# Optimization experiments

Measured on AMD Instinct MI355X. Metric: run time of the kernel, lower is better.

Reference implementation:

```python
import jax, jax.numpy as jnp
import numpy as np

K = 8  # args.k


def setup_inputs() -> dict:
    key = jax.random.key(0)
    k1, k2, k3 = jax.random.split(key, 3)
    b, n_pre, n_cur = 1, 8192, 16384
    pre_xyzs = jax.random.normal(k1, (b, 3, n_pre), dtype=jnp.float32)
    cur_xyzs = jax.random.normal(k2, (b, 3, n_cur), dtype=jnp.float32)
    # UpsampleNumLayer output range: sigmoid * (max_upsample_num - 1) + 1  in [1, 8]
    upsample_num = jax.random.uniform(k3, (b, n_pre), dtype=jnp.float32) * 7.0 + 1.0
    return {"pre_xyzs": pre_xyzs, "cur_xyzs": cur_xyzs, "upsample_num": upsample_num}


def _sqdist(a, b):
    # a: (b, n, 3), b: (b, m, 3) -> (b, n, m) squared euclidean distances
    return ((a * a).sum(-1)[:, :, None]
            + (b * b).sum(-1)[:, None, :]
            - 2.0 * jnp.einsum('bnc,bmc->bnm', a, b))


def reference(pre_xyzs, cur_xyzs, upsample_num):
    # pre_xyzs: (b, 3, n_pre); cur_xyzs: (b, 3, n_cur); upsample_num: (b, n_pre)
    pre_t = pre_xyzs.transpose(0, 2, 1)  # (b, n_pre, 3)
    cur_t = cur_xyzs.transpose(0, 2, 1)  # (b, n_cur, 3)

    # knnquery_heap(1, pre, cur): nearest pre index for each cur point -> (b, n_cur)
    cur2pre = jnp.argmin(_sqdist(cur_t, pre_t), axis=-1)

    # knnquery_heap(K, cur, pre): K nearest cur indices for each pre point -> (b, n_pre, K)
    _, knn_idx = jax.lax.top_k(-_sqdist(pre_t, cur_t), K)

    # real_center: gather cur2pre at knn_idx -> (b, n_pre, K)
    real_center = jax.vmap(lambda c2p, idx: c2p[idx])(cur2pre, knn_idx)
    expect_center = jnp.arange(pre_xyzs.shape[2])[None, :, None]  # (1, n_pre, 1)
    mask = (expect_center == real_center).astype(pre_xyzs.dtype)  # (b, n_pre, K)

    # knn_xyzs: gather cur_xyzs columns at knn_idx -> (b, 3, n_pre, K)
    knn_xyzs = jax.vmap(lambda pts, idx: pts[:, idx])(cur_xyzs, knn_idx)

    diff = knn_xyzs - pre_xyzs[..., None]              # (b, 3, n_pre, K)
    dist = jnp.sqrt((diff * diff).sum(axis=1))         # (b, n_pre, K), L2 over channel dim
    mean_distance = (dist * mask).sum(axis=-1) / upsample_num  # (b, n_pre)
    return mean_distance
```

## Files before the change

### kernel.cpp

```cpp
#include <hip/hip_runtime.h>

#define N_PRE 8192
#define N_CUR 16384
#define KNN   8


#define MAPPED_INF 0xFF800000u

__device__ __forceinline__ unsigned key_of_bits(unsigned b) {
    return b ^ (0x80000000u | (unsigned)((int)b >> 31));
}
__device__ __forceinline__ float float_of_key(unsigned k) {
    unsigned b = k ^ (0x80000000u | ~(unsigned)((int)k >> 31));
    return __uint_as_float(b);
}

__global__ __launch_bounds__(256) void prep_kernel(
        const float* __restrict__ pre, const float* __restrict__ cur,
        float4* __restrict__ pre4, float4* __restrict__ cur4) {
    int i = blockIdx.x * 256 + threadIdx.x;
    if (i < N_CUR) {
        float x = cur[i], y = cur[N_CUR + i], z = cur[2 * N_CUR + i];
        cur4[i] = make_float4(x, y, z, fmaf(x, x, fmaf(y, y, z * z)));
    }
    if (i < N_PRE) {
        float x = pre[i], y = pre[N_PRE + i], z = pre[2 * N_PRE + i];
        pre4[i] = make_float4(-2.f * x, -2.f * y, -2.f * z,
                              fmaf(x, x, fmaf(y, y, z * z)));
    }
}

#define TILE_A 2048

__global__ __launch_bounds__(1024) void cur2pre_kernel(
        const float4* __restrict__ pre4, const float4* __restrict__ cur4,
        unsigned* __restrict__ c2p) {
    __shared__ float4 sp[TILE_A];
    const int tid  = threadIdx.x;
    const int lane = tid & 63;
    const int w    = tid >> 6;
    const int j0   = blockIdx.x * 32 + w * 2;

    const float4 c0 = cur4[j0 + 0];
    const float4 c1 = cur4[j0 + 1];

    const float INF = __int_as_float(0x7F800000);
    float b0 = INF, b1 = INF;
    int   i0 = 0,   i1 = 0;

    for (int tile = 0; tile < N_PRE; tile += TILE_A) {
        __syncthreads();
        for (int k = tid; k < TILE_A; k += 1024) sp[k] = pre4[tile + k];
        __syncthreads();

#pragma unroll 8
        for (int s = 0; s < TILE_A; s += 64) {
            float4 q = sp[s + lane];
            int idx = tile + s + lane;
            float d; bool c;
            d = fmaf(q.x, c0.x, fmaf(q.y, c0.y, fmaf(q.z, c0.z, q.w)));
            c = d < b0; b0 = c ? d : b0; i0 = c ? idx : i0;
            d = fmaf(q.x, c1.x, fmaf(q.y, c1.y, fmaf(q.z, c1.z, q.w)));
            c = d < b1; b1 = c ? d : b1; i1 = c ? idx : i1;
        }
    }

    unsigned long long v0 =
        (((unsigned long long)key_of_bits(__float_as_uint(b0))) << 32) | (unsigned)i0;
    unsigned long long v1 =
        (((unsigned long long)key_of_bits(__float_as_uint(b1))) << 32) | (unsigned)i1;
#pragma unroll
    for (int off = 32; off > 0; off >>= 1) {
        unsigned long long o;
        o = __shfl_xor(v0, off); v0 = (o < v0) ? o : v0;
        o = __shfl_xor(v1, off); v1 = (o < v1) ? o : v1;
    }
    unsigned r = (unsigned)v0;
    r = (lane == 1) ? (unsigned)v1 : r;
    if (lane < 2) c2p[j0 + lane] = r;
}

#define TILE_B 1024

__device__ __forceinline__ void pop_top8(float d, float& t8, unsigned& ld,
                                         unsigned& li, int jbase) {
    unsigned long long m = __ballot(d < t8);
    while (m) {
        int src = __ffsll(m) - 1;
        unsigned fdb = (unsigned)__builtin_amdgcn_readlane(__float_as_int(d), src);
        unsigned kd = key_of_bits(fdb);
        unsigned kj = (unsigned)(jbase + src);
        unsigned ud = (unsigned)__builtin_amdgcn_update_dpp(
            0, (int)ld, 0x111, 0xF, 0xF, false);
        unsigned uj = (unsigned)__builtin_amdgcn_update_dpp(
            0, (int)li, 0x111, 0xF, 0xF, false);
        bool hi = kd < ud;
        bool lo = kd < ld;
        ld = hi ? ud : (lo ? kd : ld);
        li = hi ? uj : (lo ? kj : li);
        unsigned k7 = (unsigned)__builtin_amdgcn_readlane((int)ld, 7);
        t8 = float_of_key(k7);
        m = (m & (m - 1)) & __ballot(d < t8);
    }
}

__global__ __launch_bounds__(512) void knn_finalize_kernel(
        const float4* __restrict__ pre4, const float4* __restrict__ cur4,
        const float* __restrict__ ups,
        const unsigned* __restrict__ c2p,
        float* __restrict__ out) {
    __shared__ float4 sc[2 * TILE_B];
    unsigned long long* mb = (unsigned long long*)sc;

    const int tid  = threadIdx.x;
    const int lane = tid & 63;
    const int w    = tid >> 6;
    const int half = w >> 2;
    const int wl   = w & 3;
    const int ia   = blockIdx.x * 8 + wl * 2;
    const int ib   = ia + 1;
    const int hbase = half * (N_CUR / 2);

    const float4 p0 = pre4[ia];
    const float4 p1 = pre4[ib];

    const float INF = __int_as_float(0x7F800000);
    unsigned ld0 = MAPPED_INF, li0 = 0, ld1 = MAPPED_INF, li1 = 0;
    float t80 = INF, t81 = INF;

    for (int tile = 0; tile < N_CUR / 2; tile += TILE_B) {
        __syncthreads();
        for (int k = tid; k < 2 * TILE_B; k += 512) {
            int hh = k >> 10;
            int kk = k & (TILE_B - 1);
            sc[k] = cur4[hh * (N_CUR / 2) + tile + kk];
        }
        __syncthreads();

#pragma unroll 4
        for (int s = 0; s < TILE_B; s += 64) {
            float4 c = sc[half * TILE_B + s + lane];
            float d0 = fmaf(p0.x, c.x, fmaf(p0.y, c.y, fmaf(p0.z, c.z, c.w)));
            float d1 = fmaf(p1.x, c.x, fmaf(p1.y, c.y, fmaf(p1.z, c.z, c.w)));
            const int jbase = hbase + tile + s;
            pop_top8(d0, t80, ld0, li0, jbase);
            pop_top8(d1, t81, ld1, li1, jbase);
        }
    }

    __syncthreads();
    if (lane < 8) {
        mb[((wl * 2 + 0) * 2 + half) * 8 + lane] =
            (((unsigned long long)ld0) << 32) | li0;
        mb[((wl * 2 + 1) * 2 + half) * 8 + lane] =
            (((unsigned long long)ld1) << 32) | li1;
    }
    __syncthreads();

    if (tid < 128) {
        const int g  = tid >> 4;
        const int t  = tid & 15;
        const int pg = blockIdx.x * 8 + g;

        unsigned long long v = (t < 8) ? mb[(g * 2 + 0) * 8 + t]
                                       : mb[(g * 2 + 1) * 8 + (15 - t)];
#pragma unroll
        for (int off = 8; off > 0; off >>= 1) {
            unsigned long long o = __shfl_xor(v, off);
            bool up = (t & off) != 0;
            v = up ? ((o > v) ? o : v) : ((o < v) ? o : v);
        }

        float acc = 0.f;
        if (t < 8) {
            unsigned j = (unsigned)v;
            float4 cc = cur4[j];
            float4 pp = pre4[pg];
            float px = -0.5f * pp.x, py = -0.5f * pp.y, pz = -0.5f * pp.z;
            float dx = cc.x - px, dy = cc.y - py, dz = cc.z - pz;
            float dsq = fmaf(dx, dx, fmaf(dy, dy, dz * dz));
            acc = (c2p[j] == (unsigned)pg) ? sqrtf(dsq) : 0.f;
        }
        acc += __shfl_xor(acc, 1);
        acc += __shfl_xor(acc, 2);
        acc += __shfl_xor(acc, 4);
        if (t == 0) out[pg] = acc / ups[pg];
    }
}

extern "C" void kernel_launch(void* const* d_in, const int* in_sizes, int n_in,
                              void* d_out, int out_size, void* d_ws, size_t ws_size,
                              hipStream_t stream) {
    const float* pre = (const float*)d_in[0];
    const float* cur = (const float*)d_in[1];
    const float* ups = (const float*)d_in[2];
    float* out = (float*)d_out;

    char* ws = (char*)d_ws;
    unsigned* c2p = (unsigned*)ws;
    float4*   pre4 = (float4*)(ws + 65536);
    float4*   cur4 = (float4*)(ws + 65536 + 131072);

    prep_kernel<<<N_CUR / 256, 256, 0, stream>>>(pre, cur, pre4, cur4);

    cur2pre_kernel<<<N_CUR / 32, 1024, 0, stream>>>(pre4, cur4, c2p);

    knn_finalize_kernel<<<N_PRE / 8, 512, 0, stream>>>(pre4, cur4, ups, c2p, out);
}
```

Measured before the change: 135.6 us.

## Give each KNN wave four query points over the full candidate set

The KNN kernel is reorganised so each wave tracks top-8 lists for four pre points across all cur points. Previously each wave handled two points over half the candidates, and the two halves were merged in shared memory with a bitonic step. This removes the merge and its extra barriers, doubles the shared tile size, and prefetches the next LDS element into registers. The cost is four times fewer waves in total, which lowers occupancy for the latency-bound serial ballot/readlane insertion loops.

```diff
diff --git a/kernel.cpp b/kernel.cpp
--- a/kernel.cpp
+++ b/kernel.cpp
@@ -80,7 +80,7 @@
     if (lane < 2) c2p[j0 + lane] = r;
 }
 
-#define TILE_B 1024
+#define TILE_B 2048
 
 __device__ __forceinline__ void pop_top8(float d, float& t8, unsigned& ld,
                                          unsigned& li, int jbase) {
@@ -104,87 +104,74 @@
     }
 }
 
-__global__ __launch_bounds__(512) void knn_finalize_kernel(
+__global__ __launch_bounds__(256) void knn_finalize_kernel(
         const float4* __restrict__ pre4, const float4* __restrict__ cur4,
         const float* __restrict__ ups,
         const unsigned* __restrict__ c2p,
         float* __restrict__ out) {
-    __shared__ float4 sc[2 * TILE_B];
-    unsigned long long* mb = (unsigned long long*)sc;
-
+    __shared__ float4 sc[TILE_B];
     const int tid  = threadIdx.x;
     const int lane = tid & 63;
     const int w    = tid >> 6;
-    const int half = w >> 2;
-    const int wl   = w & 3;
-    const int ia   = blockIdx.x * 8 + wl * 2;
-    const int ib   = ia + 1;
-    const int hbase = half * (N_CUR / 2);
+    const int ia   = blockIdx.x * 16 + w * 4;
 
-    const float4 p0 = pre4[ia];
-    const float4 p1 = pre4[ib];
+    const float4 p0 = pre4[ia + 0];
+    const float4 p1 = pre4[ia + 1];
+    const float4 p2 = pre4[ia + 2];
+    const float4 p3 = pre4[ia + 3];
 
     const float INF = __int_as_float(0x7F800000);
     unsigned ld0 = MAPPED_INF, li0 = 0, ld1 = MAPPED_INF, li1 = 0;
-    float t80 = INF, t81 = INF;
+    unsigned ld2 = MAPPED_INF, li2 = 0, ld3 = MAPPED_INF, li3 = 0;
+    float t0 = INF, t1 = INF, t2 = INF, t3 = INF;
 
-    for (int tile = 0; tile < N_CUR / 2; tile += TILE_B) {
+    for (int tile = 0; tile < N_CUR; tile += TILE_B) {
         __syncthreads();
-        for (int k = tid; k < 2 * TILE_B; k += 512) {
-            int hh = k >> 10;
-            int kk = k & (TILE_B - 1);
-            sc[k] = cur4[hh * (N_CUR / 2) + tile + kk];
-        }
+        for (int k = tid; k < TILE_B; k += 256) sc[k] = cur4[tile + k];
         __syncthreads();
 
+        float4 c = sc[lane];
 #pragma unroll 4
         for (int s = 0; s < TILE_B; s += 64) {
-            float4 c = sc[half * TILE_B + s + lane];
+            float4 cn = sc[((s + 64) & (TILE_B - 1)) + lane];
             float d0 = fmaf(p0.x, c.x, fmaf(p0.y, c.y, fmaf(p0.z, c.z, c.w)));
             float d1 = fmaf(p1.x, c.x, fmaf(p1.y, c.y, fmaf(p1.z, c.z, c.w)));
-            const int jbase = hbase + tile + s;
-            pop_top8(d0, t80, ld0, li0, jbase);
-            pop_top8(d1, t81, ld1, li1, jbase);
+            float d2 = fmaf(p2.x, c.x, fmaf(p2.y, c.y, fmaf(p2.z, c.z, c.w)));
+            float d3 = fmaf(p3.x, c.x, fmaf(p3.y, c.y, fmaf(p3.z, c.z, c.w)));
+            const int jbase = tile + s;
+            pop_top8(d0, t0, ld0, li0, jbase);
+            pop_top8(d1, t1, ld1, li1, jbase);
+            pop_top8(d2, t2, ld2, li2, jbase);
+            pop_top8(d3, t3, ld3, li3, jbase);
+            c = cn;
         }
     }
 
-    __syncthreads();
-    if (lane < 8) {
-        mb[((wl * 2 + 0) * 2 + half) * 8 + lane] =
-            (((unsigned long long)ld0) << 32) | li0;
-        mb[((wl * 2 + 1) * 2 + half) * 8 + lane] =
-            (((unsigned long long)ld1) << 32) | li1;
-    }
-    __syncthreads();
+    {
+        const int row  = lane >> 4;
+        const int slot = lane & 15;
 
-    if (tid < 128) {
-        const int g  = tid >> 4;
-        const int t  = tid & 15;
-        const int pg = blockIdx.x * 8 + g;
-
-        unsigned long long v = (t < 8) ? mb[(g * 2 + 0) * 8 + t]
-                                       : mb[(g * 2 + 1) * 8 + (15 - t)];
-#pragma unroll
-        for (int off = 8; off > 0; off >>= 1) {
-            unsigned long long o = __shfl_xor(v, off);
-            bool up = (t & off) != 0;
-            v = up ? ((o > v) ? o : v) : ((o < v) ? o : v);
-        }
+        unsigned j = li0;
+        j = (row == 1) ? li1 : j;
+        j = (row == 2) ? li2 : j;
+        j = (row == 3) ? li3 : j;
 
         float acc = 0.f;
-        if (t < 8) {
-            unsigned j = (unsigned)v;
+        if (slot < 8) {
+            float4 pp = p0;
+            pp = (row == 1) ? p1 : pp;
+            pp = (row == 2) ? p2 : pp;
+            pp = (row == 3) ? p3 : pp;
             float4 cc = cur4[j];
-            float4 pp = pre4[pg];
             float px = -0.5f * pp.x, py = -0.5f * pp.y, pz = -0.5f * pp.z;
             float dx = cc.x - px, dy = cc.y - py, dz = cc.z - pz;
             float dsq = fmaf(dx, dx, fmaf(dy, dy, dz * dz));
-            acc = (c2p[j] == (unsigned)pg) ? sqrtf(dsq) : 0.f;
+            acc = (c2p[j] == (unsigned)(ia + row)) ? sqrtf(dsq) : 0.f;
         }
         acc += __shfl_xor(acc, 1);
         acc += __shfl_xor(acc, 2);
         acc += __shfl_xor(acc, 4);
-        if (t == 0) out[pg] = acc / ups[pg];
+        if (slot == 0) out[ia + row] = acc / ups[ia + row];
     }
 }
 
@@ -205,5 +192,5 @@
 
     cur2pre_kernel<<<N_CUR / 32, 1024, 0, stream>>>(pre4, cur4, c2p);
 
-    knn_finalize_kernel<<<N_PRE / 8, 512, 0, stream>>>(pre4, cur4, ups, c2p, out);
+    knn_finalize_kernel<<<N_PRE / 16, 256, 0, stream>>>(pre4, cur4, ups, c2p, out);
 }
```

New measurement: 155.7 us. 14.8% more time.
